# Kernel tuning notes

Hardware: AMD Instinct MI355X
Metric: run time of the kernel (lower is better)

## Reference

```python
import jax, jax.numpy as jnp
import numpy as np

P = 16      # patch size
DM = 512    # d_model
DI = 1024   # d_inner = expand * d_model
N = 16      # d_state
K = 4       # d_conv
DR = 32     # dt_rank = ceil(d_model/16)
NL = 8      # n_layers
NC = 1000   # num_classes


def _ln(x, w, b):
    m = x.mean(-1, keepdims=True)
    v = x.var(-1, keepdims=True)
    return (x - m) * jax.lax.rsqrt(v + 1e-5) * w + b


def _fpad(x, wl, wr, ht, hb):
    # torch F.pad(x, (wl, wr, ht, hb)) with possibly negative (crop) values, NCHW
    x = jnp.pad(x, ((0, 0), (0, 0), (max(ht, 0), max(hb, 0)), (max(wl, 0), max(wr, 0))))
    return x[:, :, -min(ht, 0):x.shape[2] + min(hb, 0), -min(wl, 0):x.shape[3] + min(wr, 0)]


def _mamba(x, in_w, conv_w, conv_b, xproj_w, dt_w, dt_b, A_log, Dp, out_w):
    # standard mamba_ssm Mamba layer; weights stored (in, out)
    B, L, _ = x.shape
    xz = x @ in_w                         # (B, L, 2*DI)
    xpart, z = xz[..., :DI], xz[..., DI:]
    # depthwise causal conv1d, kernel K, padding K-1 then truncate to L
    xc = jnp.pad(xpart.transpose(0, 2, 1), ((0, 0), (0, 0), (K - 1, 0)))  # (B, DI, L+K-1)
    conv = conv_b[None, :, None] + sum(conv_w[None, :, k, None] * xc[:, :, k:k + L] for k in range(K))
    u = jax.nn.silu(conv).transpose(0, 2, 1)    # (B, L, DI)
    dbc = u @ xproj_w                           # (B, L, DR + 2N)
    dt = jax.nn.softplus(dbc[..., :DR] @ dt_w + dt_b)  # (B, L, DI)
    Bm, Cm = dbc[..., DR:DR + N], dbc[..., DR + N:]
    A = -jnp.exp(A_log)                         # (DI, N)
    dA = jnp.exp(dt[..., None] * A)             # (B, L, DI, N)
    dBu = (dt * u)[..., None] * Bm[:, :, None, :]

    def step(h, inp):
        dA_t, dBu_t, C_t = inp
        h = dA_t * h + dBu_t                    # (B, DI, N)
        return h, jnp.einsum('bdn,bn->bd', h, C_t)

    h0 = jnp.zeros((B, DI, N), x.dtype)
    _, ys = jax.lax.scan(step, h0, (dA.transpose(1, 0, 2, 3), dBu.transpose(1, 0, 2, 3), Cm.transpose(1, 0, 2)))
    y = ys.transpose(1, 0, 2) + u * Dp          # (B, L, DI)
    return (y * jax.nn.silu(z)) @ out_w         # (B, L, DM)


def reference(img, patch_ln_w, patch_ln_b, patch_w, patch_b, pos_emb, cls_tok,
              ln_w, ln_b, in_w, conv_w, conv_b, xproj_w, dt_w, dt_b, A_log, D, out_w,
              head_ln_w, head_ln_b, head_w, head_b):
    shifts = ((1, -1, 0, 0), (-1, 1, 0, 0), (0, 0, 1, -1), (0, 0, -1, 1))
    x5 = jnp.concatenate([img] + [_fpad(img, *s) for s in shifts], axis=1)  # (B, 15, H, W)
    Bn, C, H, W = x5.shape
    # 'b c (h p1) (w p2) -> b (h w) (p1 p2 c)'
    x = x5.reshape(Bn, C, H // P, P, W // P, P).transpose(0, 2, 4, 3, 5, 1).reshape(Bn, (H // P) * (W // P), P * P * C)
    x = _ln(x, patch_ln_w, patch_ln_b) @ patch_w + patch_b  # (B, n, DM)
    n = x.shape[1]
    x = jnp.concatenate([x, jnp.broadcast_to(cls_tok, (Bn, 1, DM))], axis=1)  # cls appended at END
    x = x + pos_emb[:, :n + 1]
    for i in range(NL):
        y = _ln(x, ln_w[i], ln_b[i])
        x = x + _mamba(y, in_w[i], conv_w[i], conv_b[i], xproj_w[i], dt_w[i], dt_b[i], A_log[i], D[i], out_w[i])
    x = x[:, -1]  # pool='cls' -> last token
    return _ln(x, head_ln_w, head_ln_b) @ head_w + head_b


def setup_inputs() -> dict:
    key = jax.random.key(0)
    ks = jax.random.split(key, 12)
    B = 8
    PD = P * P * 15  # 3840
    rn = lambda k, shape, scale=1.0: jax.random.normal(k, shape, jnp.float32) * scale
    return {
        "img": rn(ks[0], (B, 3, 224, 224)),
        "patch_ln_w": jnp.ones((PD,), jnp.float32), "patch_ln_b": jnp.zeros((PD,), jnp.float32),
        "patch_w": rn(ks[1], (PD, DM), PD ** -0.5), "patch_b": jnp.zeros((DM,), jnp.float32),
        "pos_emb": rn(ks[2], (1, 197, DM), 0.02),
        "cls_tok": rn(ks[3], (1, 1, DM), 0.02),
        "ln_w": jnp.ones((NL, DM), jnp.float32), "ln_b": jnp.zeros((NL, DM), jnp.float32),
        "in_w": rn(ks[4], (NL, DM, 2 * DI), DM ** -0.5),
        "conv_w": rn(ks[5], (NL, DI, K), K ** -0.5),
        "conv_b": jnp.zeros((NL, DI), jnp.float32),
        "xproj_w": rn(ks[6], (NL, DI, DR + 2 * N), DI ** -0.5),
        "dt_w": rn(ks[7], (NL, DR, DI), DR ** -0.5),
        "dt_b": rn(ks[8], (NL, DI), 0.1) - 4.0,  # softplus -> small positive dt
        "A_log": jnp.log(jnp.broadcast_to(jnp.arange(1.0, N + 1.0, dtype=jnp.float32), (NL, DI, N))),
        "D": jnp.ones((NL, DI), jnp.float32),
        "out_w": rn(ks[9], (NL, DI, DM), DI ** -0.5),
        "head_ln_w": jnp.ones((DM,), jnp.float32), "head_ln_b": jnp.zeros((DM,), jnp.float32),
        "head_w": rn(ks[10], (DM, NC), DM ** -0.5), "head_b": jnp.zeros((NC,), jnp.float32),
    }
```

## Files before the change

kernel.cpp:

```cpp
#include <hip/hip_runtime.h>
#include <hip/hip_fp16.h>
#include <math.h>

#define BATCH   8
#define LSEQ    197
#define LPAD    200
#define NPATCH  196
#define NPTOK   (BATCH * NPATCH)
#define NTOK    (BATCH * LSEQ)
#define MPAD    1664
#define DMODEL  512
#define DINNER  1024
#define NSTATE  16
#define DRANK   32
#define NLAYER  8
#define NCLS    1000
#define PDIM    3840

typedef _Float16 f16x8 __attribute__((ext_vector_type(8)));
typedef float    f32x4 __attribute__((ext_vector_type(4)));
typedef unsigned short us8 __attribute__((ext_vector_type(8)));

__device__ __forceinline__ float f_rcp(float x) { return __builtin_amdgcn_rcpf(x); }
__device__ __forceinline__ float sp_silu(float x) { return x * f_rcp(1.0f + __expf(-x)); }
__device__ __forceinline__ float sp_softplus(float x) {
    return x > 20.0f ? x : __logf(1.0f + __expf(x));
}

#define DPP_ROW_SHR_STEP(P, NB, CTRL)                                          \
    {                                                                          \
        float t_[NB];                                                          \
        _Pragma("unroll")                                                      \
        for (int i_ = 0; i_ < NB; ++i_)                                        \
            t_[i_] = __int_as_float(__builtin_amdgcn_update_dpp(               \
                0, __float_as_int(P[i_]), CTRL, 0xF, 0xF, true));              \
        _Pragma("unroll")                                                      \
        for (int i_ = 0; i_ < NB; ++i_) P[i_] += t_[i_];                       \
    }

template <int NB>
__device__ __forceinline__ void row_sum16v(float* p) {
    DPP_ROW_SHR_STEP(p, NB, 0x111);
    DPP_ROW_SHR_STEP(p, NB, 0x112);
    DPP_ROW_SHR_STEP(p, NB, 0x114);
    DPP_ROW_SHR_STEP(p, NB, 0x118);
}

__device__ __forceinline__ void store_f16(char* __restrict__ Hb,
                                          int row, int k, int K, float v) {
    size_t byte = (size_t)row * (size_t)(K * 2) +
                  (size_t)(((unsigned)(k * 2)) ^ (unsigned)((row & 7) << 4));
    *(__half*)(Hb + byte) = __float2half_rn(v);
}

__device__ __forceinline__ void store_f16x4(char* __restrict__ Hb,
                                            int row, int k4, int K, float4 v) {
    size_t byte = (size_t)row * (size_t)(K * 2) +
                  (size_t)(((unsigned)(k4 * 2)) ^ (unsigned)((row & 7) << 4));
    *(ushort4*)(Hb + byte) = make_ushort4(
        __half_as_ushort(__float2half_rn(v.x)), __half_as_ushort(__float2half_rn(v.y)),
        __half_as_ushort(__float2half_rn(v.z)), __half_as_ushort(__float2half_rn(v.w)));
}

__device__ __forceinline__ float2 block_reduce2(float a, float b, float* lds) {
#pragma unroll
    for (int off = 32; off > 0; off >>= 1) {
        a += __shfl_down(a, off);
        b += __shfl_down(b, off);
    }
    int lane = threadIdx.x & 63, w = threadIdx.x >> 6;
    if (lane == 0) { lds[w] = a; lds[4 + w] = b; }
    __syncthreads();
    float sa = lds[0] + lds[1] + lds[2] + lds[3];
    float sb = lds[4] + lds[5] + lds[6] + lds[7];
    return make_float2(sa, sb);
}

__global__ __launch_bounds__(256) void k_patch_ln(
    const float* __restrict__ img, const float* __restrict__ lnw,
    const float* __restrict__ lnb, char* __restrict__ Xph) {
    __shared__ float vals[PDIM];
    __shared__ float red[8];
    int tok = blockIdx.x;
    int b = tok / NPATCH, p = tok % NPATCH;
    int gy = p / 14, gx = p % 14;
    int tid = threadIdx.x;
    int py = tid >> 4, px = tid & 15;
    int h0 = gy * 16 + py, w0 = gx * 16 + px;
    const int dh[5] = {0, 0, 0, -1, 1};
    const int dw[5] = {0, -1, 1, 0, 0};
    float s = 0.f, ss = 0.f;
#pragma unroll
    for (int c = 0; c < 15; ++c) {
        int g = c / 3, ch = c % 3;
        int h = h0 + dh[g], w = w0 + dw[g];
        float v = 0.f;
        if ((unsigned)h < 224u && (unsigned)w < 224u)
            v = img[((b * 3 + ch) * 224 + h) * 224 + w];
        vals[tid * 15 + c] = v;
        s += v; ss += v * v;
    }
    float2 t2 = block_reduce2(s, ss, red);
    float mean = t2.x * (1.0f / PDIM);
    float var  = t2.y * (1.0f / PDIM) - mean * mean;
    float rstd = 1.0f / sqrtf(var + 1e-5f);
    for (int j = 0; j < 15; ++j) {
        int e = tid + j * 256;
        float v = (vals[e] - mean) * rstd * lnw[e] + lnb[e];
        store_f16(Xph, tok, e, PDIM, v);
    }
}

__global__ __launch_bounds__(256) void k_ln(
    const float* __restrict__ x, const float* __restrict__ w,
    const float* __restrict__ b, char* __restrict__ yh) {
    __shared__ float red[8];
    int t = blockIdx.x, tid = threadIdx.x;
    const float* xr = x + (size_t)t * DMODEL;
    float v0 = xr[tid], v1 = xr[tid + 256];
    float2 t2 = block_reduce2(v0 + v1, v0 * v0 + v1 * v1, red);
    float mean = t2.x * (1.0f / DMODEL);
    float var  = t2.y * (1.0f / DMODEL) - mean * mean;
    float rstd = 1.0f / sqrtf(var + 1e-5f);
    store_f16(yh, t, tid,       DMODEL, (v0 - mean) * rstd * w[tid]       + b[tid]);
    store_f16(yh, t, tid + 256, DMODEL, (v1 - mean) * rstd * w[tid + 256] + b[tid + 256]);
}

__global__ __launch_bounds__(256) void k_red_ln(
    const float* __restrict__ part, float* __restrict__ xtok,
    const float* __restrict__ w, const float* __restrict__ b,
    char* __restrict__ yh) {
    __shared__ float red[8];
    int t = blockIdx.x, tid = threadIdx.x;
    size_t base = (size_t)t * DMODEL;
    float v0 = xtok[base + tid], v1 = xtok[base + tid + 256];
#pragma unroll
    for (int k = 0; k < 4; ++k) {
        v0 += part[(size_t)k * (NTOK * DMODEL) + base + tid];
        v1 += part[(size_t)k * (NTOK * DMODEL) + base + tid + 256];
    }
    xtok[base + tid] = v0;
    xtok[base + tid + 256] = v1;
    float2 t2 = block_reduce2(v0 + v1, v0 * v0 + v1 * v1, red);
    float mean = t2.x * (1.0f / DMODEL);
    float var  = t2.y * (1.0f / DMODEL) - mean * mean;
    float rstd = 1.0f / sqrtf(var + 1e-5f);
    store_f16(yh, t, tid,       DMODEL, (v0 - mean) * rstd * w[tid]       + b[tid]);
    store_f16(yh, t, tid + 256, DMODEL, (v1 - mean) * rstd * w[tid + 256] + b[tid + 256]);
}

__global__ __launch_bounds__(256) void k_wT(
    const float* __restrict__ W, char* __restrict__ Th,
    int Ks, int Ns, size_t wStride, size_t tByteStride) {
    __shared__ float t[32][33];
    int z = blockIdx.z;
    const float* Wz = W + (size_t)z * wStride;
    char* ThZ = Th + (size_t)z * tByteStride;
    int n0 = blockIdx.x * 32, k0 = blockIdx.y * 32;
    int tx = threadIdx.x, ty = threadIdx.y;
#pragma unroll
    for (int r = 0; r < 4; ++r) {
        int k = k0 + ty + r * 8, n = n0 + tx;
        t[tx][ty + r * 8] = (n < Ns) ? Wz[(size_t)k * Ns + n] : 0.f;
    }
    __syncthreads();
#pragma unroll
    for (int r = 0; r < 4; ++r) {
        int n = n0 + ty + r * 8, k = k0 + tx;
        float v = t[ty + r * 8][tx];
        size_t byte = (size_t)n * (size_t)(Ks * 2) +
                      (size_t)(((unsigned)(k * 2)) ^ (unsigned)((n & 7) << 4));
        *(__half*)(ThZ + byte) = __float2half_rn(v);
    }
}

template <bool F16OUT>
__global__ __launch_bounds__(256, 2) void k_gemm_f16(
    const char* __restrict__ Ah, const char* __restrict__ Bh,
    float* __restrict__ C, unsigned short* __restrict__ C16,
    int M, int N, int K, int kchunk, long partStride) {
    __shared__ __half L[2][2][128 * 64];
    const int tid = threadIdx.x, w = tid >> 6, lane = tid & 63;

    const int GX = gridDim.x, GY = gridDim.y;
    const int nwg = GX * GY * gridDim.z;
    const int orig = blockIdx.x + GX * (blockIdx.y + GY * blockIdx.z);
    const int q = nwg >> 3, r = nwg & 7, xcd = orig & 7, pos = orig >> 3;
    const int wrk = (xcd < r ? xcd * (q + 1) : r * (q + 1) + (xcd - r) * q) + pos;
    const int bm = wrk % GY;
    const int t1 = wrk / GY;
    const int bn = t1 % GX, bz = t1 / GX;

    const int m0 = bm * 128, n0 = bn * 128;
    const int kbeg = bz * kchunk;
    int kend = kbeg + kchunk; if (kend > K) kend = K;
    C += (size_t)bz * (size_t)partStride;
    const size_t K2 = (size_t)K * 2;
    const int srowBase = 32 * w;
    const int srLane = lane >> 3;
    const int scol = (lane & 7) * 16;

    f32x4 acc[4][4];
#pragma unroll
    for (int i = 0; i < 4; ++i)
#pragma unroll
        for (int j = 0; j < 4; ++j) acc[i][j] = (f32x4)(0.f);

    auto STAGE = [&](int buf, int k0) {
#pragma unroll
        for (int t = 0; t < 4; ++t) {
            int lr = srowBase + 8 * t;
            size_t ao = (size_t)(m0 + lr + srLane) * K2 + (size_t)k0 * 2 + scol;
            size_t bo = (size_t)(n0 + lr + srLane) * K2 + (size_t)k0 * 2 + scol;
            __builtin_amdgcn_global_load_lds(
                (const __attribute__((address_space(1))) void*)(Ah + ao),
                (__attribute__((address_space(3))) void*)&L[buf][0][lr * 64], 16, 0, 0);
            __builtin_amdgcn_global_load_lds(
                (const __attribute__((address_space(1))) void*)(Bh + bo),
                (__attribute__((address_space(3))) void*)&L[buf][1][lr * 64], 16, 0, 0);
        }
    };

    const int wr = (w >> 1) * 64, wc = (w & 1) * 64;
    const int g = lane >> 4, rr = lane & 15;
    const int nk = (kend - kbeg + 63) / 64;

    STAGE(0, kbeg);
    asm volatile("s_waitcnt vmcnt(0)" ::: "memory");
    __syncthreads();

    for (int t = 0; t < nk; ++t) {
        int cur = t & 1;
        if (t + 1 < nk) STAGE(cur ^ 1, kbeg + (t + 1) * 64);
        const __half* LA = L[cur][0];
        const __half* LB = L[cur][1];
#pragma unroll
        for (int kk = 0; kk < 2; ++kk) {
            f16x8 af[4], bf[4];
#pragma unroll
            for (int mf = 0; mf < 4; ++mf) {
                int row = wr + mf * 16 + rr;
                int off = row * 128 + ((kk * 64 + g * 16) ^ ((row & 7) << 4));
                af[mf] = *(const f16x8*)((const char*)LA + off);
            }
#pragma unroll
            for (int nf = 0; nf < 4; ++nf) {
                int row = wc + nf * 16 + rr;
                int off = row * 128 + ((kk * 64 + g * 16) ^ ((row & 7) << 4));
                bf[nf] = *(const f16x8*)((const char*)LB + off);
            }
#pragma unroll
            for (int mf = 0; mf < 4; ++mf)
#pragma unroll
                for (int nf = 0; nf < 4; ++nf)
                    acc[mf][nf] = __builtin_amdgcn_mfma_f32_16x16x32_f16(
                        af[mf], bf[nf], acc[mf][nf], 0, 0, 0);
        }
        asm volatile("s_waitcnt vmcnt(0)" ::: "memory");
        __syncthreads();
    }

#pragma unroll
    for (int mf = 0; mf < 4; ++mf)
#pragma unroll
        for (int nf = 0; nf < 4; ++nf)
#pragma unroll
            for (int e = 0; e < 4; ++e) {
                int gm = m0 + wr + mf * 16 + g * 4 + e;
                int gn = n0 + wc + nf * 16 + rr;
                if (gm < M && gn < N) {
                    if (F16OUT)
                        C16[(size_t)gm * N + gn] =
                            __half_as_ushort(__float2half_rn(acc[mf][nf][e]));
                    else
                        C[(size_t)gm * N + gn] = acc[mf][nf][e];
                }
            }
}

template <int SK, bool ACC>
__global__ __launch_bounds__(256) void k_reduce(
    const float* __restrict__ part, float* __restrict__ out, int total, int stride) {
    int i = blockIdx.x * 256 + threadIdx.x;
    if (i >= total) return;
    float s = 0.f;
#pragma unroll
    for (int k = 0; k < SK; ++k) s += part[(size_t)k * stride + i];
    out[i] = ACC ? out[i] + s : s;
}

__global__ __launch_bounds__(256) void k_assemble(
    const float* __restrict__ Pe, const float* __restrict__ patch_b,
    const float* __restrict__ cls, const float* __restrict__ pos,
    float* __restrict__ xtok) {
    int idx = blockIdx.x * 256 + threadIdx.x;
    if (idx >= NTOK * DMODEL) return;
    int d = idx % DMODEL;
    int t = (idx / DMODEL) % LSEQ;
    int b = idx / (DMODEL * LSEQ);
    float v = (t < NPATCH) ? (Pe[((size_t)b * NPATCH + t) * DMODEL + d] + patch_b[d])
                           : cls[d];
    xtok[idx] = v + pos[t * DMODEL + d];
}

__global__ __launch_bounds__(256) void k_conv(
    const unsigned short* __restrict__ xzH, const float* __restrict__ cw,
    const float* __restrict__ cb, char* __restrict__ uh) {
    int idx = blockIdx.x * 256 + threadIdx.x;
    if (idx >= NTOK * (DINNER / 4)) return;
    int dq = idx & (DINNER / 4 - 1);
    int t  = idx / (DINNER / 4);
    int l  = t % LSEQ;
    int d  = dq * 4;
    float4 w0 = *(const float4*)&cw[(d + 0) * 4];
    float4 w1 = *(const float4*)&cw[(d + 1) * 4];
    float4 w2 = *(const float4*)&cw[(d + 2) * 4];
    float4 w3 = *(const float4*)&cw[(d + 3) * 4];
    float4 acc = *(const float4*)&cb[d];
#pragma unroll
    for (int j = 0; j < 4; ++j) {
        int ls = l - 3 + j;
        if (ls >= 0) {
            union { ushort4 v; __half h[4]; } xu;
            xu.v = *(const ushort4*)&xzH[(size_t)(t - 3 + j) * (2 * DINNER) + d];
            acc.x += (&w0.x)[j] * __half2float(xu.h[0]);
            acc.y += (&w1.x)[j] * __half2float(xu.h[1]);
            acc.z += (&w2.x)[j] * __half2float(xu.h[2]);
            acc.w += (&w3.x)[j] * __half2float(xu.h[3]);
        }
    }
    float4 uv = make_float4(sp_silu(acc.x), sp_silu(acc.y),
                            sp_silu(acc.z), sp_silu(acc.w));
    store_f16x4(uh, t, d, DINNER, uv);
}

__global__ __launch_bounds__(256) void k_scan2(
    const char* __restrict__ uH, const float* __restrict__ dbc,
    const float* __restrict__ dtw, const float* __restrict__ dtb,
    const float* __restrict__ Alog, const float* __restrict__ Dp,
    const unsigned short* __restrict__ xzH, char* __restrict__ gh) {
    __shared__ float uS[LPAD * 16];
    __shared__ float dS[LPAD * 16];
    __shared__ float bS[LPAD * 16];
    __shared__ float cS[LPAD * 16];
    __shared__ float wS[DRANK * 16];
    const int tid = threadIdx.x;
    const int b = blockIdx.y, d0 = blockIdx.x * 16;

    for (int i = tid; i < DRANK * 16; i += 256)
        wS[i] = dtw[(size_t)(i >> 4) * DINNER + d0 + (i & 15)];
    __syncthreads();

    for (int i = tid; i < LPAD * 2; i += 256) {
        int l = i >> 1, jj = i & 1;
        float* dst = &uS[l * 16 + jj * 8];
        if (l >= LSEQ) {
#pragma unroll
            for (int e = 0; e < 8; ++e) dst[e] = 0.f;
            continue;
        }
        int t = b * LSEQ + l;
        size_t byte = (size_t)t * (DINNER * 2) +
                      (size_t)(((unsigned)(d0 * 2 + jj * 16)) ^ (unsigned)((t & 7) << 4));
        union { us8 v; __half h[8]; } uu;
        uu.v = *(const us8*)(uH + byte);
#pragma unroll
        for (int e = 0; e < 8; ++e) dst[e] = __half2float(uu.h[e]);
    }

    const float* dbcB = dbc + ((size_t)b * LSEQ) * 64;
    for (int i = tid; i < LPAD * 4; i += 256) {
        int l = i >> 2, j = (i & 3) << 2;
        if (l >= LSEQ) {
            float4 z = make_float4(0.f, 0.f, 0.f, 0.f);
            *(float4*)&dS[l * 16 + j] = z;
            *(float4*)&bS[l * 16 + j] = z;
            *(float4*)&cS[l * 16 + j] = z;
            continue;
        }
        *(float4*)&bS[l * 16 + j] = *(const float4*)&dbcB[(size_t)l * 64 + DRANK + j];
        *(float4*)&cS[l * 16 + j] = *(const float4*)&dbcB[(size_t)l * 64 + DRANK + 16 + j];
        float4 acc = *(const float4*)&dtb[d0 + j];
#pragma unroll
        for (int kq = 0; kq < DRANK / 4; ++kq) {
            float4 r4 = *(const float4*)&dbcB[(size_t)l * 64 + kq * 4];
#pragma unroll
            for (int m = 0; m < 4; ++m) {
                float rv = (&r4.x)[m];
                float4 w4 = *(const float4*)&wS[(kq * 4 + m) * 16 + j];
                acc.x += rv * w4.x; acc.y += rv * w4.y;
                acc.z += rv * w4.z; acc.w += rv * w4.w;
            }
        }
        dS[l * 16 + j + 0] = sp_softplus(acc.x);
        dS[l * 16 + j + 1] = sp_softplus(acc.y);
        dS[l * 16 + j + 2] = sp_softplus(acc.z);
        dS[l * 16 + j + 3] = sp_softplus(acc.w);
    }
    const int n = tid & 15, dsub = tid >> 4;
    const int d = d0 + dsub;
    const float A  = -__expf(Alog[d * NSTATE + n]);
    const float Dv = Dp[d];
    __syncthreads();

    float hn = 0.f;
    float dtc[8], uvc[8], Bnc[8], Cnc[8];
#pragma unroll
    for (int i = 0; i < 8; ++i) {
        int o = i * 16;
        dtc[i] = dS[o + dsub]; uvc[i] = uS[o + dsub];
        Bnc[i] = bS[o + n];    Cnc[i] = cS[o + n];
    }
    for (int lb = 0; lb < LPAD; lb += 8) {
        float dtN[8], uvN[8], BnN[8], CnN[8];
        if (lb + 8 < LPAD) {
#pragma unroll
            for (int i = 0; i < 8; ++i) {
                int o = (lb + 8 + i) * 16;
                dtN[i] = dS[o + dsub]; uvN[i] = uS[o + dsub];
                BnN[i] = bS[o + n];    CnN[i] = cS[o + n];
            }
        } else {
#pragma unroll
            for (int i = 0; i < 8; ++i) { dtN[i] = uvN[i] = BnN[i] = CnN[i] = 0.f; }
        }
        float a8[8], b8[8], p8[8];
#pragma unroll
        for (int i = 0; i < 8; ++i) {
            a8[i] = __expf(dtc[i] * A);
            b8[i] = dtc[i] * uvc[i] * Bnc[i];
        }
#pragma unroll
        for (int i = 0; i < 8; ++i) {
            hn = a8[i] * hn + b8[i];
            p8[i] = hn * Cnc[i];
        }
        row_sum16v<8>(p8);
#pragma unroll
        for (int i = 0; i < 8; ++i)
            if (n == 15) dS[(lb + i) * 16 + dsub] = p8[i] + uvc[i] * Dv;
#pragma unroll
        for (int i = 0; i < 8; ++i) {
            dtc[i] = dtN[i]; uvc[i] = uvN[i]; Bnc[i] = BnN[i]; Cnc[i] = CnN[i];
        }
    }
    __syncthreads();

    for (int i = tid; i < LSEQ * 4; i += 256) {
        int l = i >> 2, j = (i & 3) << 2;
        int t = b * LSEQ + l;
        union { ushort4 v; __half h[4]; } zu;
        zu.v = *(const ushort4*)&xzH[(size_t)t * (2 * DINNER) + DINNER + d0 + j];
        float4 g4 = make_float4(
            dS[l * 16 + j + 0] * sp_silu(__half2float(zu.h[0])),
            dS[l * 16 + j + 1] * sp_silu(__half2float(zu.h[1])),
            dS[l * 16 + j + 2] * sp_silu(__half2float(zu.h[2])),
            dS[l * 16 + j + 3] * sp_silu(__half2float(zu.h[3])));
        store_f16x4(gh, t, d0 + j, DINNER, g4);
    }
}

__global__ __launch_bounds__(256) void k_head(
    const float* __restrict__ xtok, const float* __restrict__ lnw,
    const float* __restrict__ lnb, const float* __restrict__ hw,
    const float* __restrict__ hb, float* __restrict__ out) {
    __shared__ float red[8];
    __shared__ float xr[DMODEL];
    int b = blockIdx.y, tid = threadIdx.x;
    const float* row = xtok + ((size_t)(b * LSEQ + NPATCH)) * DMODEL;
    float v0 = row[tid], v1 = row[tid + 256];
    float2 t2 = block_reduce2(v0 + v1, v0 * v0 + v1 * v1, red);
    float mean = t2.x * (1.0f / DMODEL);
    float var  = t2.y * (1.0f / DMODEL) - mean * mean;
    float rstd = 1.0f / sqrtf(var + 1e-5f);
    xr[tid]       = (v0 - mean) * rstd * lnw[tid] + lnb[tid];
    xr[tid + 256] = (v1 - mean) * rstd * lnw[tid + 256] + lnb[tid + 256];
    __syncthreads();
    int c = blockIdx.x * 256 + tid;
    if (c < NCLS) {
        float acc = hb[c];
#pragma unroll 8
        for (int k = 0; k < DMODEL; ++k) acc += xr[k] * hw[k * NCLS + c];
        out[b * NCLS + c] = acc;
    }
}

extern "C" void kernel_launch(void* const* d_in, const int* in_sizes, int n_in,
                              void* d_out, int out_size, void* d_ws, size_t ws_size,
                              hipStream_t stream) {
    const float* img     = (const float*)d_in[0];
    const float* plnw    = (const float*)d_in[1];
    const float* plnb    = (const float*)d_in[2];
    const float* patch_w = (const float*)d_in[3];
    const float* patch_b = (const float*)d_in[4];
    const float* pos     = (const float*)d_in[5];
    const float* cls     = (const float*)d_in[6];
    const float* ln_w    = (const float*)d_in[7];
    const float* ln_b    = (const float*)d_in[8];
    const float* in_w    = (const float*)d_in[9];
    const float* conv_w  = (const float*)d_in[10];
    const float* conv_b  = (const float*)d_in[11];
    const float* xproj   = (const float*)d_in[12];
    const float* dt_w    = (const float*)d_in[13];
    const float* dt_b    = (const float*)d_in[14];
    const float* A_log   = (const float*)d_in[15];
    const float* Dp      = (const float*)d_in[16];
    const float* out_w   = (const float*)d_in[17];
    const float* hlnw    = (const float*)d_in[18];
    const float* hlnb    = (const float*)d_in[19];
    const float* head_w  = (const float*)d_in[20];
    const float* head_b  = (const float*)d_in[21];
    float* out = (float*)d_out;

    char* p = (char*)d_ws;
    auto alloc = [&](size_t bytes) { char* r = p; p += (bytes + 255) & ~(size_t)255; return r; };
    float* xtok = (float*)alloc((size_t)NTOK * DMODEL * 4);
    unsigned short* xzH = (unsigned short*)alloc((size_t)NTOK * 2 * DINNER * 2);
    float* dbc  = (float*)alloc((size_t)NTOK * 64 * 4);
    float* Pe   = (float*)alloc((size_t)NPTOK * DMODEL * 4);
    float* part = (float*)alloc((size_t)4 * NTOK * DMODEL * 4);
    char* ylnH = alloc((size_t)MPAD * DMODEL * 2);
    char* uH   = alloc((size_t)MPAD * DINNER * 2);
    char* gH   = alloc((size_t)MPAD * DINNER * 2);
    char* XpH  = alloc((size_t)MPAD * PDIM * 2);
    char* inTH  = alloc((size_t)NLAYER * 2 * DINNER * DMODEL * 2);
    char* outTH = alloc((size_t)NLAYER * DMODEL * DINNER * 2);
    char* patTH = alloc((size_t)DMODEL * PDIM * 2);
    char* xprTH = alloc((size_t)NLAYER * 128 * DINNER * 2);

    const size_t IN_T_B  = (size_t)2 * DINNER * DMODEL * 2;
    const size_t OUT_T_B = (size_t)DMODEL * DINNER * 2;
    const size_t XPR_T_B = (size_t)128 * DINNER * 2;

    k_wT<<<dim3(2 * DINNER / 32, DMODEL / 32, NLAYER), dim3(32, 8), 0, stream>>>(
        in_w, inTH, DMODEL, 2 * DINNER, (size_t)DMODEL * 2 * DINNER, IN_T_B);
    k_wT<<<dim3(DMODEL / 32, DINNER / 32, NLAYER), dim3(32, 8), 0, stream>>>(
        out_w, outTH, DINNER, DMODEL, (size_t)DINNER * DMODEL, OUT_T_B);
    k_wT<<<dim3(DMODEL / 32, PDIM / 32, 1), dim3(32, 8), 0, stream>>>(
        patch_w, patTH, PDIM, DMODEL, 0, 0);
    k_wT<<<dim3(128 / 32, DINNER / 32, NLAYER), dim3(32, 8), 0, stream>>>(
        xproj, xprTH, DINNER, 64, (size_t)DINNER * 64, XPR_T_B);

    k_patch_ln<<<NPTOK, 256, 0, stream>>>(img, plnw, plnb, XpH);
    k_gemm_f16<false><<<dim3(4, 13, 4), 256, 0, stream>>>(
        XpH, patTH, part, nullptr, NPTOK, DMODEL, PDIM, 960, (long)NPTOK * DMODEL);
    k_reduce<4, false><<<(NPTOK * DMODEL + 255) / 256, 256, 0, stream>>>(
        part, Pe, NPTOK * DMODEL, NPTOK * DMODEL);
    k_assemble<<<(NTOK * DMODEL + 255) / 256, 256, 0, stream>>>(Pe, patch_b, cls, pos, xtok);

    for (int i = 0; i < NLAYER; ++i) {
        if (i == 0) {
            k_ln<<<NTOK, 256, 0, stream>>>(xtok, ln_w, ln_b, ylnH);
        } else {
            k_red_ln<<<NTOK, 256, 0, stream>>>(part, xtok, ln_w + i * DMODEL,
                                               ln_b + i * DMODEL, ylnH);
        }
        k_gemm_f16<true><<<dim3(16, 13, 1), 256, 0, stream>>>(
            ylnH, inTH + i * IN_T_B, nullptr, xzH, NTOK, 2 * DINNER, DMODEL, DMODEL, 0);
        k_conv<<<(NTOK * (DINNER / 4) + 255) / 256, 256, 0, stream>>>(
            xzH, conv_w + (size_t)i * DINNER * 4, conv_b + (size_t)i * DINNER, uH);
        k_gemm_f16<false><<<dim3(1, 13, 8), 256, 0, stream>>>(
            uH, xprTH + i * XPR_T_B, part, nullptr, NTOK, 64, DINNER, 128, (long)NTOK * 64);
        k_reduce<8, false><<<(NTOK * 64 + 255) / 256, 256, 0, stream>>>(
            part, dbc, NTOK * 64, NTOK * 64);
        k_scan2<<<dim3(DINNER / 16, BATCH), 256, 0, stream>>>(
            uH, dbc, dt_w + (size_t)i * DRANK * DINNER, dt_b + (size_t)i * DINNER,
            A_log + (size_t)i * DINNER * NSTATE, Dp + (size_t)i * DINNER,
            xzH, gH);
        k_gemm_f16<false><<<dim3(4, 13, 4), 256, 0, stream>>>(
            gH, outTH + i * OUT_T_B, part, nullptr, NTOK, DMODEL, DINNER, 256,
            (long)NTOK * DMODEL);
    }
    k_reduce<4, true><<<(NTOK * DMODEL + 255) / 256, 256, 0, stream>>>(
        part, xtok, NTOK * DMODEL, NTOK * DMODEL);

    k_head<<<dim3((NCLS + 255) / 256, BATCH), 256, 0, stream>>>(
        xtok, hlnw, hlnb, head_w, head_b, out);
}
```

Before: 614.5 us.

## Overlap GEMM tile loads with compute and split-K the classifier head

In the f16 GEMM main loop, the blocking wait after each tile is replaced by a partial vmcnt(8) wait issued after the next tile's loads start, together with raw s_barrier calls. The intent is to let global-to-LDS prefetch overlap the MFMA work. Separately, the final full-token residual reduction is dropped: only the 8 class-token rows are summed, inside a new head layernorm kernel. The head matmul is split over K into 8 slices across more blocks, followed by a small reduction kernel. Risks are vmcnt correctness with s_barrier lacking a full fence, and two extra launches.

```diff
diff --git a/kernel.cpp b/kernel.cpp
--- a/kernel.cpp
+++ b/kernel.cpp
@@ -226,12 +226,16 @@
     const int nk = (kend - kbeg + 63) / 64;
 
     STAGE(0, kbeg);
-    asm volatile("s_waitcnt vmcnt(0)" ::: "memory");
-    __syncthreads();
 
     for (int t = 0; t < nk; ++t) {
         int cur = t & 1;
-        if (t + 1 < nk) STAGE(cur ^ 1, kbeg + (t + 1) * 64);
+        if (t + 1 < nk) {
+            STAGE(cur ^ 1, kbeg + (t + 1) * 64);
+            asm volatile("s_waitcnt vmcnt(8)" ::: "memory");
+        } else {
+            asm volatile("s_waitcnt vmcnt(0)" ::: "memory");
+        }
+        __builtin_amdgcn_s_barrier();
         const __half* LA = L[cur][0];
         const __half* LB = L[cur][1];
 #pragma unroll
@@ -256,8 +260,7 @@
                     acc[mf][nf] = __builtin_amdgcn_mfma_f32_16x16x32_f16(
                         af[mf], bf[nf], acc[mf][nf], 0, 0, 0);
         }
-        asm volatile("s_waitcnt vmcnt(0)" ::: "memory");
-        __syncthreads();
+        __builtin_amdgcn_s_barrier();
     }
 
 #pragma unroll
@@ -460,29 +463,53 @@
     }
 }
 
-__global__ __launch_bounds__(256) void k_head(
-    const float* __restrict__ xtok, const float* __restrict__ lnw,
-    const float* __restrict__ lnb, const float* __restrict__ hw,
-    const float* __restrict__ hb, float* __restrict__ out) {
+__global__ __launch_bounds__(256) void k_head_ln(
+    const float* __restrict__ part, const float* __restrict__ xtok,
+    const float* __restrict__ lnw, const float* __restrict__ lnb,
+    float* __restrict__ xr) {
     __shared__ float red[8];
-    __shared__ float xr[DMODEL];
-    int b = blockIdx.y, tid = threadIdx.x;
-    const float* row = xtok + ((size_t)(b * LSEQ + NPATCH)) * DMODEL;
-    float v0 = row[tid], v1 = row[tid + 256];
+    int b = blockIdx.x, tid = threadIdx.x;
+    size_t base = ((size_t)(b * LSEQ + NPATCH)) * DMODEL;
+    float v0 = xtok[base + tid], v1 = xtok[base + tid + 256];
+#pragma unroll
+    for (int k = 0; k < 4; ++k) {
+        v0 += part[(size_t)k * (NTOK * DMODEL) + base + tid];
+        v1 += part[(size_t)k * (NTOK * DMODEL) + base + tid + 256];
+    }
     float2 t2 = block_reduce2(v0 + v1, v0 * v0 + v1 * v1, red);
     float mean = t2.x * (1.0f / DMODEL);
     float var  = t2.y * (1.0f / DMODEL) - mean * mean;
     float rstd = 1.0f / sqrtf(var + 1e-5f);
-    xr[tid]       = (v0 - mean) * rstd * lnw[tid] + lnb[tid];
-    xr[tid + 256] = (v1 - mean) * rstd * lnw[tid + 256] + lnb[tid + 256];
+    xr[b * DMODEL + tid]       = (v0 - mean) * rstd * lnw[tid] + lnb[tid];
+    xr[b * DMODEL + tid + 256] = (v1 - mean) * rstd * lnw[tid + 256] + lnb[tid + 256];
+}
+
+__global__ __launch_bounds__(256) void k_head_fc(
+    const float* __restrict__ xr, const float* __restrict__ hw,
+    float* __restrict__ hpart) {
+    __shared__ float xs[64];
+    int tid = threadIdx.x;
+    int c = blockIdx.x * 256 + tid;
+    int b = blockIdx.y, ks = blockIdx.z;
+    if (tid < 64) xs[tid] = xr[b * DMODEL + ks * 64 + tid];
     __syncthreads();
-    int c = blockIdx.x * 256 + tid;
-    if (c < NCLS) {
-        float acc = hb[c];
+    if (c >= NCLS) return;
+    float acc = 0.f;
 #pragma unroll 8
-        for (int k = 0; k < DMODEL; ++k) acc += xr[k] * hw[k * NCLS + c];
-        out[b * NCLS + c] = acc;
-    }
+    for (int k = 0; k < 64; ++k) acc += xs[k] * hw[(size_t)(ks * 64 + k) * NCLS + c];
+    hpart[(size_t)(ks * BATCH + b) * NCLS + c] = acc;
+}
+
+__global__ __launch_bounds__(256) void k_head_red(
+    const float* __restrict__ hpart, const float* __restrict__ hb,
+    float* __restrict__ out) {
+    int i = blockIdx.x * 256 + threadIdx.x;
+    if (i >= BATCH * NCLS) return;
+    int b = i / NCLS, c = i % NCLS;
+    float s = hb[c];
+#pragma unroll
+    for (int ks = 0; ks < 8; ++ks) s += hpart[(size_t)(ks * BATCH + b) * NCLS + c];
+    out[i] = s;
 }
 
 extern "C" void kernel_launch(void* const* d_in, const int* in_sizes, int n_in,
@@ -519,6 +546,8 @@
     float* dbc  = (float*)alloc((size_t)NTOK * 64 * 4);
     float* Pe   = (float*)alloc((size_t)NPTOK * DMODEL * 4);
     float* part = (float*)alloc((size_t)4 * NTOK * DMODEL * 4);
+    float* xr   = (float*)alloc((size_t)BATCH * DMODEL * 4);
+    float* hpart= (float*)alloc((size_t)8 * BATCH * NCLS * 4);
     char* ylnH = alloc((size_t)MPAD * DMODEL * 2);
     char* uH   = alloc((size_t)MPAD * DINNER * 2);
     char* gH   = alloc((size_t)MPAD * DINNER * 2);
@@ -571,9 +600,8 @@
             gH, outTH + i * OUT_T_B, part, nullptr, NTOK, DMODEL, DINNER, 256,
             (long)NTOK * DMODEL);
     }
-    k_reduce<4, true><<<(NTOK * DMODEL + 255) / 256, 256, 0, stream>>>(
-        part, xtok, NTOK * DMODEL, NTOK * DMODEL);
-
-    k_head<<<dim3((NCLS + 255) / 256, BATCH), 256, 0, stream>>>(
-        xtok, hlnw, hlnb, head_w, head_b, out);
-}
+
+    k_head_ln<<<BATCH, 256, 0, stream>>>(part, xtok, hlnw, hlnb, xr);
+    k_head_fc<<<dim3(4, BATCH, 8), 256, 0, stream>>>(xr, head_w, hpart);
+    k_head_red<<<(BATCH * NCLS + 255) / 256, 256, 0, stream>>>(hpart, head_b, out);
+}
```

Result: faster. 574.4 us (-6.5%).
